# Performance work log

Measured on AMD Instinct MI355X. Metric: run time of the kernel, lower is better.

## Reference

```python
import jax, jax.numpy as jnp
import numpy as np

N, K, C = 10000, 64, 128


def setup_inputs() -> dict:
    key = jax.random.key(0)
    ks = jax.random.split(key, 6)
    return {
        "real": jax.random.normal(ks[0], (N, C), dtype=jnp.float32),
        "imag": jax.random.normal(ks[1], (N, C), dtype=jnp.float32),
        "Qreal": jax.random.normal(ks[2], (N, K), dtype=jnp.float32) / np.sqrt(N),
        "Qimag": jax.random.normal(ks[3], (N, K), dtype=jnp.float32) / np.sqrt(N),
        "Ritz": jax.random.uniform(ks[4], (K,), dtype=jnp.float32),
        "weight": jax.random.normal(ks[5], (C, C), dtype=jnp.float32) * np.sqrt(2.0 / (C + C)),  # xavier-ish scale
        "long_diff": 5,
    }


def reference(real, imag, Qreal, Qimag, Ritz, weight, long_diff):
    # TT = Ritz ** long_diff ; spectral filters L = Q diag(TT) Q^H split into real/imag
    TT = jnp.power(Ritz, long_diff)  # [K]
    QrT = Qreal * TT  # [N,K] columns scaled by TT (== Qreal @ diag(TT))
    QiT = Qimag * TT
    L_real = QrT @ Qreal.T + QiT @ Qimag.T  # [N,N]
    L_imag = QiT @ Qreal.T - QrT @ Qimag.T  # [N,N]
    # complex spmm + shared dense weight: (L @ X_complex) @ W
    res_real = (L_real @ real - L_imag @ imag) @ weight  # [N,C]
    res_imag = (L_imag @ real + L_real @ imag) @ weight  # [N,C]
    # complex ReLU: mask by sign of real part
    mask = (res_real >= 0).astype(res_real.dtype)
    return real + mask * res_real, imag + mask * res_imag
```

## Files before the change

### kernel.cpp

```cpp
#include <hip/hip_runtime.h>

#define NN 10000
#define KK 64
#define CC 128
#define OUTOFF (NN * CC)
#define NA 256
#define CHUNKS_A 625

__device__ __forceinline__ float4 f4fma(float s, float4 v, float4 a) {
    a.x = fmaf(s, v.x, a.x); a.y = fmaf(s, v.y, a.y);
    a.z = fmaf(s, v.z, a.z); a.w = fmaf(s, v.w, a.w);
    return a;
}
__device__ __forceinline__ float4 f4add(float4 a, float4 b) {
    a.x += b.x; a.y += b.y; a.z += b.z; a.w += b.w; return a;
}


__global__ __launch_bounds__(512) void kA(const float* __restrict__ re,
                                          const float* __restrict__ im,
                                          const float* __restrict__ Qr,
                                          const float* __restrict__ Qi,
                                          float* __restrict__ part)
{
    __shared__ float4 smem[1536];
    const int t = threadIdx.x;
    const int bid = blockIdx.x;
    const int kt = t & 15;
    const int ctA = t >> 4;
    const int row_q = (t & 255) >> 4, q_q = t & 15;
    const int row_x = t >> 5,          q_x = t & 31;
    const float4* gq  = (const float4*)((t < 256) ? Qr : Qi);
    const float4* gre = (const float4*)re;
    const float4* gim = (const float4*)im;

    float aU[4][4] = {}, aV[4][4] = {};

    int cb = bid;
    float4 r0 = gq [(size_t)(cb * 16 + row_q) * 16 + q_q];
    float4 r1 = gre[(size_t)(cb * 16 + row_x) * 32 + q_x];
    float4 r2 = gim[(size_t)(cb * 16 + row_x) * 32 + q_x];

    while (true) {
        smem[t] = r0; smem[512 + t] = r1; smem[1024 + t] = r2;
        __syncthreads();
        const int nx = cb + NA;
        if (nx < CHUNKS_A) {
            const int m0 = nx * 16;
            r0 = gq [(size_t)(m0 + row_q) * 16 + q_q];
            r1 = gre[(size_t)(m0 + row_x) * 32 + q_x];
            r2 = gim[(size_t)(m0 + row_x) * 32 + q_x];
        }
#pragma unroll 4
        for (int rr = 0; rr < 16; ++rr) {
            float4 q_r = smem[rr * 16 + kt];
            float4 q_i = smem[256 + rr * 16 + kt];
            float4 x_r = smem[512 + rr * 32 + ctA];
            float4 x_i = smem[1024 + rr * 32 + ctA];
            float qr_[4] = {q_r.x, q_r.y, q_r.z, q_r.w};
            float qi_[4] = {q_i.x, q_i.y, q_i.z, q_i.w};
            float xr_[4] = {x_r.x, x_r.y, x_r.z, x_r.w};
            float xi_[4] = {x_i.x, x_i.y, x_i.z, x_i.w};
#pragma unroll
            for (int a = 0; a < 4; ++a)
#pragma unroll
                for (int b = 0; b < 4; ++b) {
                    aU[a][b] = fmaf(qr_[a], xr_[b], aU[a][b]);
                    aU[a][b] = fmaf(qi_[a], xi_[b], aU[a][b]);
                    aV[a][b] = fmaf(qi_[a], xr_[b], aV[a][b]);
                    aV[a][b] = fmaf(-qr_[a], xi_[b], aV[a][b]);
                }
        }
        __syncthreads();
        if (nx >= CHUNKS_A) break;
        cb = nx;
    }
    float* base = part + (size_t)bid * 16384;
    const int k0 = kt * 4, c0 = ctA * 4;
#pragma unroll
    for (int a = 0; a < 4; ++a) {
        *(float4*)(base + (k0 + a) * CC + c0)        = make_float4(aU[a][0], aU[a][1], aU[a][2], aU[a][3]);
        *(float4*)(base + 8192 + (k0 + a) * CC + c0) = make_float4(aV[a][0], aV[a][1], aV[a][2], aV[a][3]);
    }
}

__global__ __launch_bounds__(256) void kRB(const float* __restrict__ part,
                                           const float* __restrict__ Ritz,
                                           const int* __restrict__ ldp,
                                           const float* __restrict__ W,
                                           float* __restrict__ UVW)
{
    __shared__ float4 red4[256];
    __shared__ float rowS[128];
    const int t = threadIdx.x;
    const int m = blockIdx.x >> 6, k = blockIdx.x & 63;
    const int q = t & 31, sl = t >> 5;

    const float4* p = (const float4*)part + (size_t)sl * 4096 + m * 2048 + k * 32 + q;
    float4 z = make_float4(0.f, 0.f, 0.f, 0.f);
    float4 s0 = z, s1 = z, s2 = z, s3 = z;
#pragma unroll 2
    for (int jj = 0; jj < 8; ++jj) {
        s0 = f4add(s0, p[0]);
        s1 = f4add(s1, p[(size_t)8  * 4096]);
        s2 = f4add(s2, p[(size_t)16 * 4096]);
        s3 = f4add(s3, p[(size_t)24 * 4096]);
        p += (size_t)32 * 4096;
    }
    red4[t] = f4add(f4add(s0, s1), f4add(s2, s3));
    __syncthreads();
    if (t < 32) {
        float4 tot = z;
#pragma unroll
        for (int g = 0; g < 8; ++g) tot = f4add(tot, red4[g * 32 + t]);
        ((float4*)rowS)[t] = tot;
    }
    __syncthreads();
    if (t < 128) {
        float acc = 0.f;
#pragma unroll 8
        for (int cp = 0; cp < 128; ++cp)
            acc = fmaf(rowS[cp], W[cp * 128 + t], acc);
        const int ld = *ldp;
        const float rz = Ritz[k];
        float tt = 1.f;
        for (int i = 0; i < ld; ++i) tt *= rz;
        UVW[m * 8192 + k * 128 + t] = tt * acc;
    }
}

__global__ __launch_bounds__(256) void kC(const float* __restrict__ re,
                                          const float* __restrict__ im,
                                          const float* __restrict__ Qr,
                                          const float* __restrict__ Qi,
                                          const float* __restrict__ UVW,
                                          float* __restrict__ out)
{
    __shared__ float4 s[4096];
    const int t = threadIdx.x;
    {
        const float4* g = (const float4*)UVW;
        for (int i = t; i < 4096; i += 256) s[i] = g[i];
    }
    __syncthreads();
    const int ct = t & 31;
    const int r  = t >> 5;
    const int na = blockIdx.x * 16 + r;
    const int nb = na + 8;

    const float4* qra = (const float4*)(Qr + (size_t)na * KK);
    const float4* qia = (const float4*)(Qi + (size_t)na * KK);
    const float4* qrb = (const float4*)(Qr + (size_t)nb * KK);
    const float4* qib = (const float4*)(Qi + (size_t)nb * KK);

    float4 z = make_float4(0.f, 0.f, 0.f, 0.f);
    float4 Ra = z, Ia = z, Rb = z, Ib = z;

#pragma unroll 4
    for (int k4 = 0; k4 < 16; ++k4) {
        float4 QRa = qra[k4], QIa = qia[k4];
        float4 QRb = qrb[k4], QIb = qib[k4];
        float ar[4] = {QRa.x, QRa.y, QRa.z, QRa.w};
        float ai[4] = {QIa.x, QIa.y, QIa.z, QIa.w};
        float br[4] = {QRb.x, QRb.y, QRb.z, QRb.w};
        float bi[4] = {QIb.x, QIb.y, QIb.z, QIb.w};
#pragma unroll
        for (int j = 0; j < 4; ++j) {
            const int k = k4 * 4 + j;
            float4 uw = s[k * 32 + ct];
            float4 vw = s[2048 + k * 32 + ct];
            Ra = f4fma(ar[j], uw, Ra); Ra = f4fma(ai[j], vw, Ra);
            Ia = f4fma(ai[j], uw, Ia); Ia = f4fma(-ar[j], vw, Ia);
            Rb = f4fma(br[j], uw, Rb); Rb = f4fma(bi[j], vw, Rb);
            Ib = f4fma(bi[j], uw, Ib); Ib = f4fma(-br[j], vw, Ib);
        }
    }
    const int cc = ct * 4;
    {
        float4 rin = *(const float4*)(re + (size_t)na * CC + cc);
        float4 iin = *(const float4*)(im + (size_t)na * CC + cc);
        float4 orr, oii;
        orr.x = rin.x + (Ra.x >= 0.f ? Ra.x : 0.f); oii.x = iin.x + (Ra.x >= 0.f ? Ia.x : 0.f);
        orr.y = rin.y + (Ra.y >= 0.f ? Ra.y : 0.f); oii.y = iin.y + (Ra.y >= 0.f ? Ia.y : 0.f);
        orr.z = rin.z + (Ra.z >= 0.f ? Ra.z : 0.f); oii.z = iin.z + (Ra.z >= 0.f ? Ia.z : 0.f);
        orr.w = rin.w + (Ra.w >= 0.f ? Ra.w : 0.f); oii.w = iin.w + (Ra.w >= 0.f ? Ia.w : 0.f);
        *(float4*)(out + (size_t)na * CC + cc)          = orr;
        *(float4*)(out + OUTOFF + (size_t)na * CC + cc) = oii;
    }
    {
        float4 rin = *(const float4*)(re + (size_t)nb * CC + cc);
        float4 iin = *(const float4*)(im + (size_t)nb * CC + cc);
        float4 orr, oii;
        orr.x = rin.x + (Rb.x >= 0.f ? Rb.x : 0.f); oii.x = iin.x + (Rb.x >= 0.f ? Ib.x : 0.f);
        orr.y = rin.y + (Rb.y >= 0.f ? Rb.y : 0.f); oii.y = iin.y + (Rb.y >= 0.f ? Ib.y : 0.f);
        orr.z = rin.z + (Rb.z >= 0.f ? Rb.z : 0.f); oii.z = iin.z + (Rb.z >= 0.f ? Ib.z : 0.f);
        orr.w = rin.w + (Rb.w >= 0.f ? Rb.w : 0.f); oii.w = iin.w + (Rb.w >= 0.f ? Ib.w : 0.f);
        *(float4*)(out + (size_t)nb * CC + cc)          = orr;
        *(float4*)(out + OUTOFF + (size_t)nb * CC + cc) = oii;
    }
}

extern "C" void kernel_launch(void* const* d_in, const int* in_sizes, int n_in,
                              void* d_out, int out_size, void* d_ws, size_t ws_size,
                              hipStream_t stream) {
    const float* re   = (const float*)d_in[0];
    const float* im   = (const float*)d_in[1];
    const float* Qr   = (const float*)d_in[2];
    const float* Qi   = (const float*)d_in[3];
    const float* Ritz = (const float*)d_in[4];
    const float* W    = (const float*)d_in[5];
    const int*   ldp  = (const int*)d_in[6];
    float* out = (float*)d_out;
    float* ws  = (float*)d_ws;

    float* part = ws;
    float* UVW  = ws + (size_t)NA * 16384;

    kA <<<NA,  512, 0, stream>>>(re, im, Qr, Qi, part);
    kRB<<<128, 256, 0, stream>>>(part, Ritz, ldp, W, UVW);
    kC <<<625, 256, 0, stream>>>(re, im, Qr, Qi, UVW, out);
}
```

Before: 114.3 us.

## Fuse the three stage kernels into one cooperative kernel with grid syncs

Merges the partial projection, the reduction plus weight multiply, and the output expansion into one persistent cooperative kernel of 256 blocks. The stages are separated by grid.sync() instead of separate launches. The aim is to remove two launch boundaries and their tail and drain gaps. In exchange, the final stage reads the UVW table straight from global/L2 rather than staging it in LDS. It also handles one row per thread instead of two, and the cooperative launch and grid barriers add their own overhead.

```diff
diff --git a/kernel.cpp b/kernel.cpp
--- a/kernel.cpp
+++ b/kernel.cpp
@@ -1,4 +1,7 @@
 #include <hip/hip_runtime.h>
+#include <hip/hip_cooperative_groups.h>
+
+namespace cg = cooperative_groups;
 
 #define NN 10000
 #define KK 64
@@ -17,186 +20,155 @@
 }
 
 
-__global__ __launch_bounds__(512) void kA(const float* __restrict__ re,
-                                          const float* __restrict__ im,
-                                          const float* __restrict__ Qr,
-                                          const float* __restrict__ Qi,
-                                          float* __restrict__ part)
+__global__ __launch_bounds__(512) void kFused(
+        const float* __restrict__ re, const float* __restrict__ im,
+        const float* __restrict__ Qr, const float* __restrict__ Qi,
+        const float* __restrict__ Ritz, const float* __restrict__ W,
+        const int* __restrict__ ldp,
+        float* __restrict__ out, float* __restrict__ ws)
 {
     __shared__ float4 smem[1536];
+    cg::grid_group grid = cg::this_grid();
     const int t = threadIdx.x;
     const int bid = blockIdx.x;
-    const int kt = t & 15;
-    const int ctA = t >> 4;
-    const int row_q = (t & 255) >> 4, q_q = t & 15;
-    const int row_x = t >> 5,          q_x = t & 31;
-    const float4* gq  = (const float4*)((t < 256) ? Qr : Qi);
-    const float4* gre = (const float4*)re;
-    const float4* gim = (const float4*)im;
+    float* part = ws;
+    float* UVW  = ws + (size_t)NA * 16384;
 
-    float aU[4][4] = {}, aV[4][4] = {};
+    {
+        const int kt = t & 15;
+        const int ctA = t >> 4;
+        const int row_q = (t & 255) >> 4, q_q = t & 15;
+        const int row_x = t >> 5,          q_x = t & 31;
+        const float4* gq  = (const float4*)((t < 256) ? Qr : Qi);
+        const float4* gre = (const float4*)re;
+        const float4* gim = (const float4*)im;
 
-    int cb = bid;
-    float4 r0 = gq [(size_t)(cb * 16 + row_q) * 16 + q_q];
-    float4 r1 = gre[(size_t)(cb * 16 + row_x) * 32 + q_x];
-    float4 r2 = gim[(size_t)(cb * 16 + row_x) * 32 + q_x];
+        float aU[4][4] = {}, aV[4][4] = {};
+        int cb = bid;
+        float4 r0 = gq [(size_t)(cb * 16 + row_q) * 16 + q_q];
+        float4 r1 = gre[(size_t)(cb * 16 + row_x) * 32 + q_x];
+        float4 r2 = gim[(size_t)(cb * 16 + row_x) * 32 + q_x];
 
-    while (true) {
-        smem[t] = r0; smem[512 + t] = r1; smem[1024 + t] = r2;
+        while (true) {
+            smem[t] = r0; smem[512 + t] = r1; smem[1024 + t] = r2;
+            __syncthreads();
+            const int nx = cb + NA;
+            if (nx < CHUNKS_A) {
+                const int m0 = nx * 16;
+                r0 = gq [(size_t)(m0 + row_q) * 16 + q_q];
+                r1 = gre[(size_t)(m0 + row_x) * 32 + q_x];
+                r2 = gim[(size_t)(m0 + row_x) * 32 + q_x];
+            }
+#pragma unroll 4
+            for (int rr = 0; rr < 16; ++rr) {
+                float4 q_r = smem[rr * 16 + kt];
+                float4 q_i = smem[256 + rr * 16 + kt];
+                float4 x_r = smem[512 + rr * 32 + ctA];
+                float4 x_i = smem[1024 + rr * 32 + ctA];
+                float qr_[4] = {q_r.x, q_r.y, q_r.z, q_r.w};
+                float qi_[4] = {q_i.x, q_i.y, q_i.z, q_i.w};
+                float xr_[4] = {x_r.x, x_r.y, x_r.z, x_r.w};
+                float xi_[4] = {x_i.x, x_i.y, x_i.z, x_i.w};
+#pragma unroll
+                for (int a = 0; a < 4; ++a)
+#pragma unroll
+                    for (int b = 0; b < 4; ++b) {
+                        aU[a][b] = fmaf(qr_[a], xr_[b], aU[a][b]);
+                        aU[a][b] = fmaf(qi_[a], xi_[b], aU[a][b]);
+                        aV[a][b] = fmaf(qi_[a], xr_[b], aV[a][b]);
+                        aV[a][b] = fmaf(-qr_[a], xi_[b], aV[a][b]);
+                    }
+            }
+            __syncthreads();
+            if (nx >= CHUNKS_A) break;
+            cb = nx;
+        }
+        float* base = part + (size_t)bid * 16384;
+        const int k0 = kt * 4, c0 = ctA * 4;
+#pragma unroll
+        for (int a = 0; a < 4; ++a) {
+            *(float4*)(base + (k0 + a) * CC + c0)        = make_float4(aU[a][0], aU[a][1], aU[a][2], aU[a][3]);
+            *(float4*)(base + 8192 + (k0 + a) * CC + c0) = make_float4(aV[a][0], aV[a][1], aV[a][2], aV[a][3]);
+        }
+    }
+
+    grid.sync();
+
+    if (bid < 128) {
+        float4* red4 = smem;
+        float*  rowS = (float*)(smem + 512);
+        const int m = bid >> 6, k = bid & 63;
+        const int q = t & 31, sl = t >> 5;
+        const float4* p = (const float4*)part + (size_t)sl * 4096 + m * 2048 + k * 32 + q;
+        float4 z = make_float4(0.f, 0.f, 0.f, 0.f);
+        float4 s0 = z, s1 = z, s2 = z, s3 = z;
+#pragma unroll
+        for (int i = 0; i < 4; ++i) {
+            s0 = f4add(s0, p[(size_t)(i)      * 65536]);
+            s1 = f4add(s1, p[(size_t)(i + 4)  * 65536]);
+            s2 = f4add(s2, p[(size_t)(i + 8)  * 65536]);
+            s3 = f4add(s3, p[(size_t)(i + 12) * 65536]);
+        }
+        red4[t] = f4add(f4add(s0, s1), f4add(s2, s3));
         __syncthreads();
-        const int nx = cb + NA;
-        if (nx < CHUNKS_A) {
-            const int m0 = nx * 16;
-            r0 = gq [(size_t)(m0 + row_q) * 16 + q_q];
-            r1 = gre[(size_t)(m0 + row_x) * 32 + q_x];
-            r2 = gim[(size_t)(m0 + row_x) * 32 + q_x];
-        }
-#pragma unroll 4
-        for (int rr = 0; rr < 16; ++rr) {
-            float4 q_r = smem[rr * 16 + kt];
-            float4 q_i = smem[256 + rr * 16 + kt];
-            float4 x_r = smem[512 + rr * 32 + ctA];
-            float4 x_i = smem[1024 + rr * 32 + ctA];
-            float qr_[4] = {q_r.x, q_r.y, q_r.z, q_r.w};
-            float qi_[4] = {q_i.x, q_i.y, q_i.z, q_i.w};
-            float xr_[4] = {x_r.x, x_r.y, x_r.z, x_r.w};
-            float xi_[4] = {x_i.x, x_i.y, x_i.z, x_i.w};
+        if (t < 32) {
+            float4 tot = z;
 #pragma unroll
-            for (int a = 0; a < 4; ++a)
-#pragma unroll
-                for (int b = 0; b < 4; ++b) {
-                    aU[a][b] = fmaf(qr_[a], xr_[b], aU[a][b]);
-                    aU[a][b] = fmaf(qi_[a], xi_[b], aU[a][b]);
-                    aV[a][b] = fmaf(qi_[a], xr_[b], aV[a][b]);
-                    aV[a][b] = fmaf(-qr_[a], xi_[b], aV[a][b]);
-                }
+            for (int g = 0; g < 16; ++g) tot = f4add(tot, red4[g * 32 + t]);
+            ((float4*)rowS)[t] = tot;
         }
         __syncthreads();
-        if (nx >= CHUNKS_A) break;
-        cb = nx;
-    }
-    float* base = part + (size_t)bid * 16384;
-    const int k0 = kt * 4, c0 = ctA * 4;
-#pragma unroll
-    for (int a = 0; a < 4; ++a) {
-        *(float4*)(base + (k0 + a) * CC + c0)        = make_float4(aU[a][0], aU[a][1], aU[a][2], aU[a][3]);
-        *(float4*)(base + 8192 + (k0 + a) * CC + c0) = make_float4(aV[a][0], aV[a][1], aV[a][2], aV[a][3]);
-    }
-}
-
-__global__ __launch_bounds__(256) void kRB(const float* __restrict__ part,
-                                           const float* __restrict__ Ritz,
-                                           const int* __restrict__ ldp,
-                                           const float* __restrict__ W,
-                                           float* __restrict__ UVW)
-{
-    __shared__ float4 red4[256];
-    __shared__ float rowS[128];
-    const int t = threadIdx.x;
-    const int m = blockIdx.x >> 6, k = blockIdx.x & 63;
-    const int q = t & 31, sl = t >> 5;
-
-    const float4* p = (const float4*)part + (size_t)sl * 4096 + m * 2048 + k * 32 + q;
-    float4 z = make_float4(0.f, 0.f, 0.f, 0.f);
-    float4 s0 = z, s1 = z, s2 = z, s3 = z;
-#pragma unroll 2
-    for (int jj = 0; jj < 8; ++jj) {
-        s0 = f4add(s0, p[0]);
-        s1 = f4add(s1, p[(size_t)8  * 4096]);
-        s2 = f4add(s2, p[(size_t)16 * 4096]);
-        s3 = f4add(s3, p[(size_t)24 * 4096]);
-        p += (size_t)32 * 4096;
-    }
-    red4[t] = f4add(f4add(s0, s1), f4add(s2, s3));
-    __syncthreads();
-    if (t < 32) {
-        float4 tot = z;
-#pragma unroll
-        for (int g = 0; g < 8; ++g) tot = f4add(tot, red4[g * 32 + t]);
-        ((float4*)rowS)[t] = tot;
-    }
-    __syncthreads();
-    if (t < 128) {
-        float acc = 0.f;
+        if (t < 128) {
+            float acc = 0.f;
 #pragma unroll 8
-        for (int cp = 0; cp < 128; ++cp)
-            acc = fmaf(rowS[cp], W[cp * 128 + t], acc);
-        const int ld = *ldp;
-        const float rz = Ritz[k];
-        float tt = 1.f;
-        for (int i = 0; i < ld; ++i) tt *= rz;
-        UVW[m * 8192 + k * 128 + t] = tt * acc;
-    }
-}
-
-__global__ __launch_bounds__(256) void kC(const float* __restrict__ re,
-                                          const float* __restrict__ im,
-                                          const float* __restrict__ Qr,
-                                          const float* __restrict__ Qi,
-                                          const float* __restrict__ UVW,
-                                          float* __restrict__ out)
-{
-    __shared__ float4 s[4096];
-    const int t = threadIdx.x;
-    {
-        const float4* g = (const float4*)UVW;
-        for (int i = t; i < 4096; i += 256) s[i] = g[i];
-    }
-    __syncthreads();
-    const int ct = t & 31;
-    const int r  = t >> 5;
-    const int na = blockIdx.x * 16 + r;
-    const int nb = na + 8;
-
-    const float4* qra = (const float4*)(Qr + (size_t)na * KK);
-    const float4* qia = (const float4*)(Qi + (size_t)na * KK);
-    const float4* qrb = (const float4*)(Qr + (size_t)nb * KK);
-    const float4* qib = (const float4*)(Qi + (size_t)nb * KK);
-
-    float4 z = make_float4(0.f, 0.f, 0.f, 0.f);
-    float4 Ra = z, Ia = z, Rb = z, Ib = z;
-
-#pragma unroll 4
-    for (int k4 = 0; k4 < 16; ++k4) {
-        float4 QRa = qra[k4], QIa = qia[k4];
-        float4 QRb = qrb[k4], QIb = qib[k4];
-        float ar[4] = {QRa.x, QRa.y, QRa.z, QRa.w};
-        float ai[4] = {QIa.x, QIa.y, QIa.z, QIa.w};
-        float br[4] = {QRb.x, QRb.y, QRb.z, QRb.w};
-        float bi[4] = {QIb.x, QIb.y, QIb.z, QIb.w};
-#pragma unroll
-        for (int j = 0; j < 4; ++j) {
-            const int k = k4 * 4 + j;
-            float4 uw = s[k * 32 + ct];
-            float4 vw = s[2048 + k * 32 + ct];
-            Ra = f4fma(ar[j], uw, Ra); Ra = f4fma(ai[j], vw, Ra);
-            Ia = f4fma(ai[j], uw, Ia); Ia = f4fma(-ar[j], vw, Ia);
-            Rb = f4fma(br[j], uw, Rb); Rb = f4fma(bi[j], vw, Rb);
-            Ib = f4fma(bi[j], uw, Ib); Ib = f4fma(-br[j], vw, Ib);
+            for (int cp = 0; cp < 128; ++cp)
+                acc = fmaf(rowS[cp], W[cp * 128 + t], acc);
+            const int ld = *ldp;
+            const float rz = Ritz[k];
+            float tt = 1.f;
+            for (int i = 0; i < ld; ++i) tt *= rz;
+            UVW[m * 8192 + k * 128 + t] = tt * acc;
         }
     }
-    const int cc = ct * 4;
+
+    grid.sync();
+
     {
-        float4 rin = *(const float4*)(re + (size_t)na * CC + cc);
-        float4 iin = *(const float4*)(im + (size_t)na * CC + cc);
-        float4 orr, oii;
-        orr.x = rin.x + (Ra.x >= 0.f ? Ra.x : 0.f); oii.x = iin.x + (Ra.x >= 0.f ? Ia.x : 0.f);
-        orr.y = rin.y + (Ra.y >= 0.f ? Ra.y : 0.f); oii.y = iin.y + (Ra.y >= 0.f ? Ia.y : 0.f);
-        orr.z = rin.z + (Ra.z >= 0.f ? Ra.z : 0.f); oii.z = iin.z + (Ra.z >= 0.f ? Ia.z : 0.f);
-        orr.w = rin.w + (Ra.w >= 0.f ? Ra.w : 0.f); oii.w = iin.w + (Ra.w >= 0.f ? Ia.w : 0.f);
-        *(float4*)(out + (size_t)na * CC + cc)          = orr;
-        *(float4*)(out + OUTOFF + (size_t)na * CC + cc) = oii;
-    }
-    {
-        float4 rin = *(const float4*)(re + (size_t)nb * CC + cc);
-        float4 iin = *(const float4*)(im + (size_t)nb * CC + cc);
-        float4 orr, oii;
-        orr.x = rin.x + (Rb.x >= 0.f ? Rb.x : 0.f); oii.x = iin.x + (Rb.x >= 0.f ? Ib.x : 0.f);
-        orr.y = rin.y + (Rb.y >= 0.f ? Rb.y : 0.f); oii.y = iin.y + (Rb.y >= 0.f ? Ib.y : 0.f);
-        orr.z = rin.z + (Rb.z >= 0.f ? Rb.z : 0.f); oii.z = iin.z + (Rb.z >= 0.f ? Ib.z : 0.f);
-        orr.w = rin.w + (Rb.w >= 0.f ? Rb.w : 0.f); oii.w = iin.w + (Rb.w >= 0.f ? Ib.w : 0.f);
-        *(float4*)(out + (size_t)nb * CC + cc)          = orr;
-        *(float4*)(out + OUTOFF + (size_t)nb * CC + cc) = oii;
+        const float4* U4 = (const float4*)UVW;
+        const float4* V4 = U4 + 2048;
+        const int ct = t & 31;
+        const int r  = t >> 5;
+        const float4 z = make_float4(0.f, 0.f, 0.f, 0.f);
+        for (int j = bid; j < CHUNKS_A; j += NA) {
+            const int na = j * 16 + r;
+            const float4* qr4 = (const float4*)(Qr + (size_t)na * KK);
+            const float4* qi4 = (const float4*)(Qi + (size_t)na * KK);
+            float4 Ra = z, Ia = z;
+#pragma unroll 4
+            for (int k4 = 0; k4 < 16; ++k4) {
+                float4 QR = qr4[k4], QI = qi4[k4];
+                float ar[4] = {QR.x, QR.y, QR.z, QR.w};
+                float ai[4] = {QI.x, QI.y, QI.z, QI.w};
+#pragma unroll
+                for (int jj = 0; jj < 4; ++jj) {
+                    const int k = k4 * 4 + jj;
+                    float4 uw = U4[k * 32 + ct];
+                    float4 vw = V4[k * 32 + ct];
+                    Ra = f4fma(ar[jj], uw, Ra); Ra = f4fma(ai[jj], vw, Ra);
+                    Ia = f4fma(ai[jj], uw, Ia); Ia = f4fma(-ar[jj], vw, Ia);
+                }
+            }
+            const int cc = ct * 4;
+            float4 rin = *(const float4*)(re + (size_t)na * CC + cc);
+            float4 iin = *(const float4*)(im + (size_t)na * CC + cc);
+            float4 orr, oii;
+            orr.x = rin.x + (Ra.x >= 0.f ? Ra.x : 0.f); oii.x = iin.x + (Ra.x >= 0.f ? Ia.x : 0.f);
+            orr.y = rin.y + (Ra.y >= 0.f ? Ra.y : 0.f); oii.y = iin.y + (Ra.y >= 0.f ? Ia.y : 0.f);
+            orr.z = rin.z + (Ra.z >= 0.f ? Ra.z : 0.f); oii.z = iin.z + (Ra.z >= 0.f ? Ia.z : 0.f);
+            orr.w = rin.w + (Ra.w >= 0.f ? Ra.w : 0.f); oii.w = iin.w + (Ra.w >= 0.f ? Ia.w : 0.f);
+            *(float4*)(out + (size_t)na * CC + cc)          = orr;
+            *(float4*)(out + OUTOFF + (size_t)na * CC + cc) = oii;
+        }
     }
 }
 
@@ -213,10 +185,7 @@
     float* out = (float*)d_out;
     float* ws  = (float*)d_ws;
 
-    float* part = ws;
-    float* UVW  = ws + (size_t)NA * 16384;
-
-    kA <<<NA,  512, 0, stream>>>(re, im, Qr, Qi, part);
-    kRB<<<128, 256, 0, stream>>>(part, Ritz, ldp, W, UVW);
-    kC <<<625, 256, 0, stream>>>(re, im, Qr, Qi, UVW, out);
+    void* args[] = {(void*)&re, (void*)&im, (void*)&Qr, (void*)&Qi,
+                    (void*)&Ritz, (void*)&W, (void*)&ldp, (void*)&out, (void*)&ws};
+    hipLaunchCooperativeKernel((const void*)kFused, dim3(NA), dim3(512), args, 0, stream);
 }
```

After: 205.6 us. 79.9% more time.

## Split reduction into wide partial-sum kernel and separate W-projection kernel

Applied to the files above, without the earlier changes.

kA now launches one block per 16-row chunk (625 blocks) with no persistent loop, so it writes 625 partial tiles instead of 256. The cross-block reduction is split out: kR1 sums the partials with 256 blocks of 512 threads, and kR2 applies W and the Ritz power. kC drops its 64KB shared-memory staging of UVW and reads UVW directly from global memory, relying on the cache. This raises parallelism and occupancy but adds a kernel launch, more partial-sum traffic (about 40MB written then read), and uncached-by-LDS repeated reads in kC.

```diff
diff --git a/kernel.cpp b/kernel.cpp
--- a/kernel.cpp
+++ b/kernel.cpp
@@ -4,8 +4,8 @@
 #define KK 64
 #define CC 128
 #define OUTOFF (NN * CC)
-#define NA 256
-#define CHUNKS_A 625
+#define NCH 625
+#define PART_F4 4096
 
 __device__ __forceinline__ float4 f4fma(float s, float4 v, float4 a) {
     a.x = fmaf(s, v.x, a.x); a.y = fmaf(s, v.y, a.y);
@@ -34,46 +34,31 @@
     const float4* gre = (const float4*)re;
     const float4* gim = (const float4*)im;
 
+    smem[t]        = gq [(size_t)(bid * 16 + row_q) * 16 + q_q];
+    smem[512 + t]  = gre[(size_t)(bid * 16 + row_x) * 32 + q_x];
+    smem[1024 + t] = gim[(size_t)(bid * 16 + row_x) * 32 + q_x];
+    __syncthreads();
+
     float aU[4][4] = {}, aV[4][4] = {};
-
-    int cb = bid;
-    float4 r0 = gq [(size_t)(cb * 16 + row_q) * 16 + q_q];
-    float4 r1 = gre[(size_t)(cb * 16 + row_x) * 32 + q_x];
-    float4 r2 = gim[(size_t)(cb * 16 + row_x) * 32 + q_x];
-
-    while (true) {
-        smem[t] = r0; smem[512 + t] = r1; smem[1024 + t] = r2;
-        __syncthreads();
-        const int nx = cb + NA;
-        if (nx < CHUNKS_A) {
-            const int m0 = nx * 16;
-            r0 = gq [(size_t)(m0 + row_q) * 16 + q_q];
-            r1 = gre[(size_t)(m0 + row_x) * 32 + q_x];
-            r2 = gim[(size_t)(m0 + row_x) * 32 + q_x];
-        }
 #pragma unroll 4
-        for (int rr = 0; rr < 16; ++rr) {
-            float4 q_r = smem[rr * 16 + kt];
-            float4 q_i = smem[256 + rr * 16 + kt];
-            float4 x_r = smem[512 + rr * 32 + ctA];
-            float4 x_i = smem[1024 + rr * 32 + ctA];
-            float qr_[4] = {q_r.x, q_r.y, q_r.z, q_r.w};
-            float qi_[4] = {q_i.x, q_i.y, q_i.z, q_i.w};
-            float xr_[4] = {x_r.x, x_r.y, x_r.z, x_r.w};
-            float xi_[4] = {x_i.x, x_i.y, x_i.z, x_i.w};
-#pragma unroll
-            for (int a = 0; a < 4; ++a)
-#pragma unroll
-                for (int b = 0; b < 4; ++b) {
-                    aU[a][b] = fmaf(qr_[a], xr_[b], aU[a][b]);
-                    aU[a][b] = fmaf(qi_[a], xi_[b], aU[a][b]);
-                    aV[a][b] = fmaf(qi_[a], xr_[b], aV[a][b]);
-                    aV[a][b] = fmaf(-qr_[a], xi_[b], aV[a][b]);
-                }
-        }
-        __syncthreads();
-        if (nx >= CHUNKS_A) break;
-        cb = nx;
+    for (int rr = 0; rr < 16; ++rr) {
+        float4 q_r = smem[rr * 16 + kt];
+        float4 q_i = smem[256 + rr * 16 + kt];
+        float4 x_r = smem[512 + rr * 32 + ctA];
+        float4 x_i = smem[1024 + rr * 32 + ctA];
+        float qr_[4] = {q_r.x, q_r.y, q_r.z, q_r.w};
+        float qi_[4] = {q_i.x, q_i.y, q_i.z, q_i.w};
+        float xr_[4] = {x_r.x, x_r.y, x_r.z, x_r.w};
+        float xi_[4] = {x_i.x, x_i.y, x_i.z, x_i.w};
+#pragma unroll
+        for (int a = 0; a < 4; ++a)
+#pragma unroll
+            for (int b = 0; b < 4; ++b) {
+                aU[a][b] = fmaf(qr_[a], xr_[b], aU[a][b]);
+                aU[a][b] = fmaf(qi_[a], xi_[b], aU[a][b]);
+                aV[a][b] = fmaf(qi_[a], xr_[b], aV[a][b]);
+                aV[a][b] = fmaf(-qr_[a], xi_[b], aV[a][b]);
+            }
     }
     float* base = part + (size_t)bid * 16384;
     const int k0 = kt * 4, c0 = ctA * 4;
@@ -84,49 +69,59 @@
     }
 }
 
-__global__ __launch_bounds__(256) void kRB(const float* __restrict__ part,
+__global__ __launch_bounds__(512) void kR1(const float* __restrict__ part,
+                                           float* __restrict__ row)
+{
+    __shared__ float4 red4[512];
+    const int t = threadIdx.x;
+    const int i = t & 15;
+    const int g = t >> 4;
+    const int o = blockIdx.x * 16 + i;
+    const float4* p = (const float4*)part + (size_t)g * PART_F4 + o;
+    const float4 z = make_float4(0.f, 0.f, 0.f, 0.f);
+    float4 s0 = z, s1 = z, s2 = z, s3 = z;
+    int pp = g;
+    for (; pp + 96 < NCH; pp += 128) {
+        s0 = f4add(s0, p[0]);
+        s1 = f4add(s1, p[(size_t)32 * PART_F4]);
+        s2 = f4add(s2, p[(size_t)64 * PART_F4]);
+        s3 = f4add(s3, p[(size_t)96 * PART_F4]);
+        p += (size_t)128 * PART_F4;
+    }
+    for (; pp < NCH; pp += 32) {
+        s0 = f4add(s0, p[0]);
+        p += (size_t)32 * PART_F4;
+    }
+    red4[t] = f4add(f4add(s0, s1), f4add(s2, s3));
+    __syncthreads();
+    if (t < 16) {
+        float4 tot = z;
+#pragma unroll
+        for (int gg = 0; gg < 32; ++gg) tot = f4add(tot, red4[gg * 16 + t]);
+        ((float4*)row)[blockIdx.x * 16 + t] = tot;
+    }
+}
+
+__global__ __launch_bounds__(128) void kR2(const float* __restrict__ row,
                                            const float* __restrict__ Ritz,
                                            const int* __restrict__ ldp,
                                            const float* __restrict__ W,
                                            float* __restrict__ UVW)
 {
-    __shared__ float4 red4[256];
     __shared__ float rowS[128];
     const int t = threadIdx.x;
     const int m = blockIdx.x >> 6, k = blockIdx.x & 63;
-    const int q = t & 31, sl = t >> 5;
-
-    const float4* p = (const float4*)part + (size_t)sl * 4096 + m * 2048 + k * 32 + q;
-    float4 z = make_float4(0.f, 0.f, 0.f, 0.f);
-    float4 s0 = z, s1 = z, s2 = z, s3 = z;
-#pragma unroll 2
-    for (int jj = 0; jj < 8; ++jj) {
-        s0 = f4add(s0, p[0]);
-        s1 = f4add(s1, p[(size_t)8  * 4096]);
-        s2 = f4add(s2, p[(size_t)16 * 4096]);
-        s3 = f4add(s3, p[(size_t)24 * 4096]);
-        p += (size_t)32 * 4096;
-    }
-    red4[t] = f4add(f4add(s0, s1), f4add(s2, s3));
+    rowS[t] = row[m * 8192 + k * 128 + t];
     __syncthreads();
-    if (t < 32) {
-        float4 tot = z;
-#pragma unroll
-        for (int g = 0; g < 8; ++g) tot = f4add(tot, red4[g * 32 + t]);
-        ((float4*)rowS)[t] = tot;
-    }
-    __syncthreads();
-    if (t < 128) {
-        float acc = 0.f;
+    float acc = 0.f;
 #pragma unroll 8
-        for (int cp = 0; cp < 128; ++cp)
-            acc = fmaf(rowS[cp], W[cp * 128 + t], acc);
-        const int ld = *ldp;
-        const float rz = Ritz[k];
-        float tt = 1.f;
-        for (int i = 0; i < ld; ++i) tt *= rz;
-        UVW[m * 8192 + k * 128 + t] = tt * acc;
-    }
+    for (int cp = 0; cp < 128; ++cp)
+        acc = fmaf(rowS[cp], W[cp * 128 + t], acc);
+    const int ld = *ldp;
+    const float rz = Ritz[k];
+    float tt = 1.f;
+    for (int i = 0; i < ld; ++i) tt *= rz;
+    UVW[m * 8192 + k * 128 + t] = tt * acc;
 }
 
 __global__ __launch_bounds__(256) void kC(const float* __restrict__ re,
@@ -136,17 +131,13 @@
                                           const float* __restrict__ UVW,
                                           float* __restrict__ out)
 {
-    __shared__ float4 s[4096];
-    const int t = threadIdx.x;
-    {
-        const float4* g = (const float4*)UVW;
-        for (int i = t; i < 4096; i += 256) s[i] = g[i];
-    }
-    __syncthreads();
+    const int t = threadIdx.x;
     const int ct = t & 31;
     const int r  = t >> 5;
     const int na = blockIdx.x * 16 + r;
     const int nb = na + 8;
+    const float4* U4 = (const float4*)UVW;
+    const float4* V4 = U4 + 2048;
 
     const float4* qra = (const float4*)(Qr + (size_t)na * KK);
     const float4* qia = (const float4*)(Qi + (size_t)na * KK);
@@ -165,14 +156,14 @@
         float br[4] = {QRb.x, QRb.y, QRb.z, QRb.w};
         float bi[4] = {QIb.x, QIb.y, QIb.z, QIb.w};
 #pragma unroll
-        for (int j = 0; j < 4; ++j) {
-            const int k = k4 * 4 + j;
-            float4 uw = s[k * 32 + ct];
-            float4 vw = s[2048 + k * 32 + ct];
-            Ra = f4fma(ar[j], uw, Ra); Ra = f4fma(ai[j], vw, Ra);
-            Ia = f4fma(ai[j], uw, Ia); Ia = f4fma(-ar[j], vw, Ia);
-            Rb = f4fma(br[j], uw, Rb); Rb = f4fma(bi[j], vw, Rb);
-            Ib = f4fma(bi[j], uw, Ib); Ib = f4fma(-br[j], vw, Ib);
+        for (int jj = 0; jj < 4; ++jj) {
+            const int k = k4 * 4 + jj;
+            float4 uw = U4[k * 32 + ct];
+            float4 vw = V4[k * 32 + ct];
+            Ra = f4fma(ar[jj], uw, Ra); Ra = f4fma(ai[jj], vw, Ra);
+            Ia = f4fma(ai[jj], uw, Ia); Ia = f4fma(-ar[jj], vw, Ia);
+            Rb = f4fma(br[jj], uw, Rb); Rb = f4fma(bi[jj], vw, Rb);
+            Ib = f4fma(bi[jj], uw, Ib); Ib = f4fma(-br[jj], vw, Ib);
         }
     }
     const int cc = ct * 4;
@@ -214,9 +205,11 @@
     float* ws  = (float*)d_ws;
 
     float* part = ws;
-    float* UVW  = ws + (size_t)NA * 16384;
-
-    kA <<<NA,  512, 0, stream>>>(re, im, Qr, Qi, part);
-    kRB<<<128, 256, 0, stream>>>(part, Ritz, ldp, W, UVW);
-    kC <<<625, 256, 0, stream>>>(re, im, Qr, Qi, UVW, out);
-}
+    float* row  = ws + (size_t)NCH * 16384;
+    float* UVW  = row + 16384;
+
+    kA <<<NCH, 512, 0, stream>>>(re, im, Qr, Qi, part);
+    kR1<<<256, 512, 0, stream>>>(part, row);
+    kR2<<<128, 128, 0, stream>>>(row, Ritz, ldp, W, UVW);
+    kC <<<NCH, 256, 0, stream>>>(re, im, Qr, Qi, UVW, out);
+}
```

Measured after the change: 123.1 us. 1.08x slower.

## Split K across two half-blocks in kC and read UVW from global

Applied to the files above, without the earlier changes.

kC no longer stages the whole 64KB UVW matrix into shared memory per block. Instead each block uses 512 threads, with two halves each covering half of the K range and reading UVW directly from global memory (L2/L1 cached). Partial sums are combined through a small shared exchange buffer. The aim is to remove the large per-block LDS staging load and its occupancy limit, at the cost of uncached-in-LDS repeated global reads and an extra sync.

```diff
diff --git a/kernel.cpp b/kernel.cpp
--- a/kernel.cpp
+++ b/kernel.cpp
@@ -129,35 +129,36 @@
     }
 }
 
-__global__ __launch_bounds__(256) void kC(const float* __restrict__ re,
+__global__ __launch_bounds__(512) void kC(const float* __restrict__ re,
                                           const float* __restrict__ im,
                                           const float* __restrict__ Qr,
                                           const float* __restrict__ Qi,
                                           const float* __restrict__ UVW,
                                           float* __restrict__ out)
 {
-    __shared__ float4 s[4096];
+    __shared__ float4 xch[4][256];
     const int t = threadIdx.x;
-    {
-        const float4* g = (const float4*)UVW;
-        for (int i = t; i < 4096; i += 256) s[i] = g[i];
-    }
-    __syncthreads();
     const int ct = t & 31;
-    const int r  = t >> 5;
+    const int r  = (t >> 5) & 7;
+    const int kh = t >> 8;
     const int na = blockIdx.x * 16 + r;
     const int nb = na + 8;
-
+    const int idx = r * 32 + ct;
+
+    const float4* U4 = (const float4*)UVW;
+    const float4* V4 = U4 + 2048;
     const float4* qra = (const float4*)(Qr + (size_t)na * KK);
     const float4* qia = (const float4*)(Qi + (size_t)na * KK);
     const float4* qrb = (const float4*)(Qr + (size_t)nb * KK);
     const float4* qib = (const float4*)(Qi + (size_t)nb * KK);
 
-    float4 z = make_float4(0.f, 0.f, 0.f, 0.f);
+    const float4 z = make_float4(0.f, 0.f, 0.f, 0.f);
     float4 Ra = z, Ia = z, Rb = z, Ib = z;
 
-#pragma unroll 4
-    for (int k4 = 0; k4 < 16; ++k4) {
+    const int k4base = kh * 8;
+#pragma unroll
+    for (int k4i = 0; k4i < 8; ++k4i) {
+        const int k4 = k4base + k4i;
         float4 QRa = qra[k4], QIa = qia[k4];
         float4 QRb = qrb[k4], QIb = qib[k4];
         float ar[4] = {QRa.x, QRa.y, QRa.z, QRa.w};
@@ -165,38 +166,47 @@
         float br[4] = {QRb.x, QRb.y, QRb.z, QRb.w};
         float bi[4] = {QIb.x, QIb.y, QIb.z, QIb.w};
 #pragma unroll
-        for (int j = 0; j < 4; ++j) {
-            const int k = k4 * 4 + j;
-            float4 uw = s[k * 32 + ct];
-            float4 vw = s[2048 + k * 32 + ct];
-            Ra = f4fma(ar[j], uw, Ra); Ra = f4fma(ai[j], vw, Ra);
-            Ia = f4fma(ai[j], uw, Ia); Ia = f4fma(-ar[j], vw, Ia);
-            Rb = f4fma(br[j], uw, Rb); Rb = f4fma(bi[j], vw, Rb);
-            Ib = f4fma(bi[j], uw, Ib); Ib = f4fma(-br[j], vw, Ib);
-        }
-    }
-    const int cc = ct * 4;
-    {
-        float4 rin = *(const float4*)(re + (size_t)na * CC + cc);
-        float4 iin = *(const float4*)(im + (size_t)na * CC + cc);
-        float4 orr, oii;
-        orr.x = rin.x + (Ra.x >= 0.f ? Ra.x : 0.f); oii.x = iin.x + (Ra.x >= 0.f ? Ia.x : 0.f);
-        orr.y = rin.y + (Ra.y >= 0.f ? Ra.y : 0.f); oii.y = iin.y + (Ra.y >= 0.f ? Ia.y : 0.f);
-        orr.z = rin.z + (Ra.z >= 0.f ? Ra.z : 0.f); oii.z = iin.z + (Ra.z >= 0.f ? Ia.z : 0.f);
-        orr.w = rin.w + (Ra.w >= 0.f ? Ra.w : 0.f); oii.w = iin.w + (Ra.w >= 0.f ? Ia.w : 0.f);
-        *(float4*)(out + (size_t)na * CC + cc)          = orr;
-        *(float4*)(out + OUTOFF + (size_t)na * CC + cc) = oii;
-    }
-    {
-        float4 rin = *(const float4*)(re + (size_t)nb * CC + cc);
-        float4 iin = *(const float4*)(im + (size_t)nb * CC + cc);
-        float4 orr, oii;
-        orr.x = rin.x + (Rb.x >= 0.f ? Rb.x : 0.f); oii.x = iin.x + (Rb.x >= 0.f ? Ib.x : 0.f);
-        orr.y = rin.y + (Rb.y >= 0.f ? Rb.y : 0.f); oii.y = iin.y + (Rb.y >= 0.f ? Ib.y : 0.f);
-        orr.z = rin.z + (Rb.z >= 0.f ? Rb.z : 0.f); oii.z = iin.z + (Rb.z >= 0.f ? Ib.z : 0.f);
-        orr.w = rin.w + (Rb.w >= 0.f ? Rb.w : 0.f); oii.w = iin.w + (Rb.w >= 0.f ? Ib.w : 0.f);
-        *(float4*)(out + (size_t)nb * CC + cc)          = orr;
-        *(float4*)(out + OUTOFF + (size_t)nb * CC + cc) = oii;
+        for (int jj = 0; jj < 4; ++jj) {
+            const int k = k4 * 4 + jj;
+            float4 uw = U4[k * 32 + ct];
+            float4 vw = V4[k * 32 + ct];
+            Ra = f4fma(ar[jj], uw, Ra); Ra = f4fma(ai[jj], vw, Ra);
+            Ia = f4fma(ai[jj], uw, Ia); Ia = f4fma(-ar[jj], vw, Ia);
+            Rb = f4fma(br[jj], uw, Rb); Rb = f4fma(bi[jj], vw, Rb);
+            Ib = f4fma(bi[jj], uw, Ib); Ib = f4fma(-br[jj], vw, Ib);
+        }
+    }
+    if (kh == 1) {
+        xch[0][idx] = Ra; xch[1][idx] = Ia;
+        xch[2][idx] = Rb; xch[3][idx] = Ib;
+    }
+    __syncthreads();
+    if (kh == 0) {
+        Ra = f4add(Ra, xch[0][idx]); Ia = f4add(Ia, xch[1][idx]);
+        Rb = f4add(Rb, xch[2][idx]); Ib = f4add(Ib, xch[3][idx]);
+        const int cc = ct * 4;
+        {
+            float4 rin = *(const float4*)(re + (size_t)na * CC + cc);
+            float4 iin = *(const float4*)(im + (size_t)na * CC + cc);
+            float4 orr, oii;
+            orr.x = rin.x + (Ra.x >= 0.f ? Ra.x : 0.f); oii.x = iin.x + (Ra.x >= 0.f ? Ia.x : 0.f);
+            orr.y = rin.y + (Ra.y >= 0.f ? Ra.y : 0.f); oii.y = iin.y + (Ra.y >= 0.f ? Ia.y : 0.f);
+            orr.z = rin.z + (Ra.z >= 0.f ? Ra.z : 0.f); oii.z = iin.z + (Ra.z >= 0.f ? Ia.z : 0.f);
+            orr.w = rin.w + (Ra.w >= 0.f ? Ra.w : 0.f); oii.w = iin.w + (Ra.w >= 0.f ? Ia.w : 0.f);
+            *(float4*)(out + (size_t)na * CC + cc)          = orr;
+            *(float4*)(out + OUTOFF + (size_t)na * CC + cc) = oii;
+        }
+        {
+            float4 rin = *(const float4*)(re + (size_t)nb * CC + cc);
+            float4 iin = *(const float4*)(im + (size_t)nb * CC + cc);
+            float4 orr, oii;
+            orr.x = rin.x + (Rb.x >= 0.f ? Rb.x : 0.f); oii.x = iin.x + (Rb.x >= 0.f ? Ib.x : 0.f);
+            orr.y = rin.y + (Rb.y >= 0.f ? Rb.y : 0.f); oii.y = iin.y + (Rb.y >= 0.f ? Ib.y : 0.f);
+            orr.z = rin.z + (Rb.z >= 0.f ? Rb.z : 0.f); oii.z = iin.z + (Rb.z >= 0.f ? Ib.z : 0.f);
+            orr.w = rin.w + (Rb.w >= 0.f ? Rb.w : 0.f); oii.w = iin.w + (Rb.w >= 0.f ? Ib.w : 0.f);
+            *(float4*)(out + (size_t)nb * CC + cc)          = orr;
+            *(float4*)(out + OUTOFF + (size_t)nb * CC + cc) = oii;
+        }
     }
 }
 
@@ -218,5 +228,5 @@
 
     kA <<<NA,  512, 0, stream>>>(re, im, Qr, Qi, part);
     kRB<<<128, 256, 0, stream>>>(part, Ritz, ldp, W, UVW);
-    kC <<<625, 256, 0, stream>>>(re, im, Qr, Qi, UVW, out);
-}
+    kC <<<625, 512, 0, stream>>>(re, im, Qr, Qi, UVW, out);
+}
```

Result: slower. 117.2 us (+2.6%).
